# Kernel optimization log

Hardware: AMD Instinct MI355X
Metric: run time of the kernel (lower is better)

The kernel has to match this reference:

```python
import jax, jax.numpy as jnp
import numpy as np

C = 256
C8 = C // 8
B, H, W = 4, 64, 64


def setup_inputs() -> dict:
    key = jax.random.key(0)
    ks = jax.random.split(key, 8)
    s = 0.02
    return {
        "x": jax.random.normal(ks[0], (B, C, H, W), dtype=jnp.float32),
        "qw": jax.random.normal(ks[1], (C8, C), dtype=jnp.float32) * s,
        "qb": jax.random.normal(ks[2], (C8,), dtype=jnp.float32) * s,
        "kw": jax.random.normal(ks[3], (C8, C), dtype=jnp.float32) * s,
        "kb": jax.random.normal(ks[4], (C8,), dtype=jnp.float32) * s,
        "vw": jax.random.normal(ks[5], (C, C), dtype=jnp.float32) * s,
        "vb": jax.random.normal(ks[6], (C,), dtype=jnp.float32) * s,
        "gamma": jnp.full((1,), 0.1, dtype=jnp.float32),
    }


def reference(x, qw, qb, kw, kb, vw, vb, gamma):
    b, c, h, w = x.shape
    n = h * w
    xf = x.reshape(b, c, n)  # (B, C, N)
    # 1x1 convs == per-pixel linear projections
    q = jnp.einsum('dc,bcn->bnd', qw, xf) + qb  # (B, N, C/8)
    k = jnp.einsum('dc,bcn->bdn', kw, xf) + kb[None, :, None]  # (B, C/8, N)
    v = jnp.einsum('dc,bcn->bdn', vw, xf) + vb[None, :, None]  # (B, C, N)
    scores = jnp.einsum('bnd,bdm->bnm', q, k)  # (B, N, N), no scale (as in source)
    attn = jax.nn.softmax(scores, axis=-1)
    # out[b,c,i] = sum_j v[b,c,j] * attn[b,i,j]
    out = jnp.einsum('bcj,bij->bci', v, attn).reshape(b, c, h, w)
    return x + gamma.reshape(()) * out
```

## Files before the change

kernel.cpp:

```cpp
#include <hip/hip_runtime.h>
#include <hip/hip_bf16.h>
#include <math.h>

#define CC 256
#define NN 4096

typedef __bf16 bf16x8 __attribute__((ext_vector_type(8)));
typedef __bf16 bf16x4 __attribute__((ext_vector_type(4)));
typedef float  f32x4  __attribute__((ext_vector_type(4)));

#define MFMA16x16x32 __builtin_amdgcn_mfma_f32_16x16x32_bf16

__device__ inline float exp2_hw(float x) {
    float r;
    asm("v_exp_f32 %0, %1" : "=v"(r) : "v"(x));
    return r;
}

__device__ inline int kperm(int j) {
    return ((j & 12) << 1) | ((j & 16) >> 2) | (j & 3);
}

__global__ void wprep_kernel(
    const float* __restrict__ qw, const float* __restrict__ qb,
    const float* __restrict__ kw, const float* __restrict__ kb,
    const float* __restrict__ vw, const float* __restrict__ vb,
    __bf16* __restrict__ Wh, __bf16* __restrict__ Wl, float* __restrict__ biasF)
{
    const int r = blockIdx.x;
    const int c = threadIdx.x;
    const float L2E = 1.4426950408889634f;
    const float* wsrc; const float* bsrc; int r0; float scale;
    if (r < 32)       { wsrc = qw; bsrc = qb; r0 = r;      scale = L2E; }
    else if (r < 64)  { wsrc = kw; bsrc = kb; r0 = r - 32; scale = 1.f; }
    else              { wsrc = vw; bsrc = vb; r0 = r - 64; scale = 1.f; }
    float v = wsrc[(size_t)r0 * CC + c] * scale;
    __bf16 hi = (__bf16)v;
    Wh[(size_t)r * CC + c] = hi;
    Wl[(size_t)r * CC + c] = (__bf16)(v - (float)hi);
    if (c == 0) biasF[r] = bsrc[r0] * scale;
}

__global__ __launch_bounds__(512) void proj_kernel(
    const float* __restrict__ x,
    const __bf16* __restrict__ Wh, const __bf16* __restrict__ Wl,
    const float* __restrict__ biasF,
    __bf16* __restrict__ Qb, __bf16* __restrict__ Kb, __bf16* __restrict__ V2)
{
    const int t    = threadIdx.x;
    const int w    = t >> 6;
    const int lane = t & 63;
    const int lrow = lane & 15;
    const int lgrp = lane >> 4;
    const int n0   = blockIdx.x * 64;
    const int b    = blockIdx.y;
    const int nt   = w & 3;
    const int rp   = w >> 2;

    __shared__ float  xs[64][68];
    __shared__ __bf16 xbh[64][136];
    __shared__ __bf16 xbl[64][136];

    f32x4 acc[10];
    #pragma unroll
    for (int i = 0; i < 10; ++i) acc[i] = f32x4{0.f, 0.f, 0.f, 0.f};

    for (int ch = 0; ch < 2; ++ch) {
        for (int cc = 0; cc < 2; ++cc) {
            __syncthreads();
            {
                const float* xg = x + ((size_t)b * CC + ch * 128 + cc * 64) * NN + n0;
                const int row = t >> 3;
                const int col = (t & 7) * 8;
                float4 a0 = *(const float4*)&xg[(size_t)row * NN + col];
                float4 a1 = *(const float4*)&xg[(size_t)row * NN + col + 4];
                *(float4*)&xs[row][col]     = a0;
                *(float4*)&xs[row][col + 4] = a1;
            }
            __syncthreads();
            {
                const int cn = t & 63;
                const int cg = t >> 6;
                bf16x8 h, l;
                #pragma unroll
                for (int e = 0; e < 8; ++e) {
                    float v = xs[cg * 8 + e][cn];
                    __bf16 hi = (__bf16)v;
                    h[e] = hi; l[e] = (__bf16)(v - (float)hi);
                }
                *(bf16x8*)&xbh[cn][cc * 64 + cg * 8] = h;
                *(bf16x8*)&xbl[cn][cc * 64 + cg * 8] = l;
            }
        }
        __syncthreads();

        #pragma unroll
        for (int ks = 0; ks < 4; ++ks) {
            const bf16x8 bh = *(const bf16x8*)&xbh[nt * 16 + lrow][ks * 32 + lgrp * 8];
            const bf16x8 bl = *(const bf16x8*)&xbl[nt * 16 + lrow][ks * 32 + lgrp * 8];
            #pragma unroll
            for (int i = 0; i < 10; ++i) {
                const int rt = rp + 2 * i;
                const size_t ao = (size_t)(rt * 16 + lrow) * CC + ch * 128 + ks * 32 + lgrp * 8;
                const bf16x8 ah = *(const bf16x8*)&Wh[ao];
                const bf16x8 al = *(const bf16x8*)&Wl[ao];
                acc[i] = MFMA16x16x32(ah, bh, acc[i], 0, 0, 0);
                acc[i] = MFMA16x16x32(ah, bl, acc[i], 0, 0, 0);
                acc[i] = MFMA16x16x32(al, bh, acc[i], 0, 0, 0);
            }
        }
    }

    const int n = n0 + nt * 16 + lrow;
    #pragma unroll
    for (int i = 0; i < 10; ++i) {
        const int rt = rp + 2 * i;
        const int g0 = rt * 16 + lgrp * 4;
        const float4 b4 = *(const float4*)&biasF[g0];
        const float v0 = acc[i].x + b4.x, v1 = acc[i].y + b4.y;
        const float v2 = acc[i].z + b4.z, v3 = acc[i].w + b4.w;
        if (g0 < 32) {
            bf16x4 o = { (__bf16)v0, (__bf16)v1, (__bf16)v2, (__bf16)v3 };
            *(bf16x4*)&Qb[((size_t)b * NN + n) * 32 + g0] = o;
        } else if (g0 < 64) {
            bf16x4 o = { (__bf16)v0, (__bf16)v1, (__bf16)v2, (__bf16)v3 };
            *(bf16x4*)&Kb[((size_t)b * NN + n) * 32 + (g0 - 32)] = o;
        } else {
            const int c = g0 - 64;
            const size_t base = ((size_t)b * 128 + (n >> 5)) * (CC * 32) + kperm(n & 31);
            V2[base + (size_t)(c + 0) * 32] = (__bf16)v0;
            V2[base + (size_t)(c + 1) * 32] = (__bf16)v1;
            V2[base + (size_t)(c + 2) * 32] = (__bf16)v2;
            V2[base + (size_t)(c + 3) * 32] = (__bf16)v3;
        }
    }
}

__global__ __launch_bounds__(512, 2) void attn_kernel(
    const __bf16* __restrict__ Qb, const __bf16* __restrict__ Kb,
    const __bf16* __restrict__ V2,
    const float* __restrict__ x, const float* __restrict__ gamma,
    float* __restrict__ y)
{
    const int bid  = blockIdx.x;
    const int xcd  = bid & 7;
    const int b    = xcd >> 1;
    const int qt   = (xcd & 1) * 32 + (bid >> 3);
    const int w    = threadIdx.x >> 6;
    const int lane = threadIdx.x & 63;
    const int lrow = lane & 15;
    const int lgrp = lane >> 4;
    const int qg   = w >> 1;
    const int kh   = w & 1;
    const int c0w  = w * 32;

    __shared__ __align__(16) __bf16 P[2][64][64];
    __shared__ float lsumP[64][2];

    const __bf16* Qbb = Qb + (size_t)b * NN * 32;
    const __bf16* Kbb = Kb + (size_t)b * NN * 32;
    const __bf16* Vbb = V2 + (size_t)b * 128 * (CC * 32);

    const bf16x8 qf = *(const bf16x8*)&Qbb[(size_t)(qt * 64 + qg * 16 + lrow) * 32 + lgrp * 8];

    const size_t koff0 = (size_t)(kh * 32 + lrow) * 32 + lgrp * 8;
    const size_t koff1 = koff0 + 16 * 32;
    const size_t vbase = (size_t)(c0w + lrow) * 32 + lgrp * 8;

    f32x4 Oa[4], Ob[4];
    #pragma unroll
    for (int g2 = 0; g2 < 4; ++g2) { Oa[g2] = f32x4{0.f,0.f,0.f,0.f}; Ob[g2] = f32x4{0.f,0.f,0.f,0.f}; }
    float lsum_l = 0.f;
    const f32x4 zf = f32x4{0.f, 0.f, 0.f, 0.f};

    const int swz  = 16 * (lrow & 7);
    char* prow_w   = (char*)&P[0][qg * 16 + lrow][0];
    const int woff = (kh * 64 + 16 * lgrp) ^ swz;

    bf16x8 kf0 = *(const bf16x8*)&Kbb[koff0];
    bf16x8 kf1 = *(const bf16x8*)&Kbb[koff1];

    for (int jt = 0; jt < 64; ++jt) {
        const size_t vrow = ((size_t)(2 * jt)) * (CC * 32) + vbase;
        const bf16x8 vf00 = *(const bf16x8*)&Vbb[vrow];
        const bf16x8 vf01 = *(const bf16x8*)&Vbb[vrow + 16 * 32];
        const bf16x8 vf10 = *(const bf16x8*)&Vbb[vrow + (size_t)(CC * 32)];
        const bf16x8 vf11 = *(const bf16x8*)&Vbb[vrow + (size_t)(CC * 32) + 16 * 32];
        const size_t jn = (size_t)((jt + 1) & 63) * 64 * 32;
        const bf16x8 kn0 = *(const bf16x8*)&Kbb[jn + koff0];
        const bf16x8 kn1 = *(const bf16x8*)&Kbb[jn + koff1];

        const f32x4 s0 = MFMA16x16x32(kf0, qf, zf, 0, 0, 0);
        const f32x4 s1 = MFMA16x16x32(kf1, qf, zf, 0, 0, 0);

        float ps = 0.f;
        bf16x8 pk;
        #pragma unroll
        for (int r = 0; r < 4; ++r) { float e = exp2_hw(s0[r]); ps += e; pk[r]     = (__bf16)e; }
        #pragma unroll
        for (int r = 0; r < 4; ++r) { float e = exp2_hw(s1[r]); ps += e; pk[4 + r] = (__bf16)e; }
        lsum_l += ps;

        const int buf = jt & 1;
        *(bf16x8*)(prow_w + buf * 8192 + woff) = pk;

        asm volatile("s_waitcnt lgkmcnt(0)\n\ts_barrier" ::: "memory");

        #pragma unroll
        for (int g2 = 0; g2 < 4; ++g2) {
            const char* prow_r = (const char*)&P[buf][g2 * 16 + lrow][0];
            const bf16x8 pb0 = *(const bf16x8*)(prow_r + ((16 * lgrp) ^ swz));
            const bf16x8 pb1 = *(const bf16x8*)(prow_r + ((64 + 16 * lgrp) ^ swz));
            Oa[g2] = MFMA16x16x32(vf00, pb0, Oa[g2], 0, 0, 0);
            Oa[g2] = MFMA16x16x32(vf10, pb1, Oa[g2], 0, 0, 0);
            Ob[g2] = MFMA16x16x32(vf01, pb0, Ob[g2], 0, 0, 0);
            Ob[g2] = MFMA16x16x32(vf11, pb1, Ob[g2], 0, 0, 0);
        }
        kf0 = kn0; kf1 = kn1;
    }

    lsum_l += __shfl_xor(lsum_l, 16);
    lsum_l += __shfl_xor(lsum_l, 32);
    if (lgrp == 0) lsumP[qg * 16 + lrow][kh] = lsum_l;
    __syncthreads();

    const float gm = gamma[0];
    #pragma unroll
    for (int g2 = 0; g2 < 4; ++g2) {
        const int q = qt * 64 + g2 * 16 + lrow;
        const float rinv = 1.f / (lsumP[g2 * 16 + lrow][0] + lsumP[g2 * 16 + lrow][1]);
        #pragma unroll
        for (int r = 0; r < 4; ++r) {
            const int c0 = c0w + lgrp * 4 + r;
            const size_t i0 = ((size_t)b * CC + c0) * NN + q;
            y[i0] = x[i0] + gm * Oa[g2][r] * rinv;
            const size_t i1 = ((size_t)b * CC + c0 + 16) * NN + q;
            y[i1] = x[i1] + gm * Ob[g2][r] * rinv;
        }
    }
}

extern "C" void kernel_launch(void* const* d_in, const int* in_sizes, int n_in,
                              void* d_out, int out_size, void* d_ws, size_t ws_size,
                              hipStream_t stream)
{
    const float* x     = (const float*)d_in[0];
    const float* qw    = (const float*)d_in[1];
    const float* qb    = (const float*)d_in[2];
    const float* kw    = (const float*)d_in[3];
    const float* kb    = (const float*)d_in[4];
    const float* vw    = (const float*)d_in[5];
    const float* vb    = (const float*)d_in[6];
    const float* gamma = (const float*)d_in[7];
    float* y = (float*)d_out;

    char* ws = (char*)d_ws;
    __bf16* Wh    = (__bf16*)(ws);
    __bf16* Wl    = (__bf16*)(ws + 163840);
    float*  biasF = (float*) (ws + 327680);
    __bf16* Qb    = (__bf16*)(ws + 1048576);
    __bf16* Kb    = (__bf16*)(ws + 2097152);
    __bf16* V2    = (__bf16*)(ws + 3145728);

    hipLaunchKernelGGL(wprep_kernel, dim3(320), dim3(256), 0, stream,
                       qw, qb, kw, kb, vw, vb, Wh, Wl, biasF);
    hipLaunchKernelGGL(proj_kernel, dim3(64, 4), dim3(512), 0, stream,
                       x, Wh, Wl, biasF, Qb, Kb, V2);
    hipLaunchKernelGGL(attn_kernel, dim3(256), dim3(512), 0, stream,
                       Qb, Kb, V2, x, gamma, y);
}
```

Measured before the change: 178.2 us.

## Split projection rows and attention channels across twice as many blocks

The projection kernel now splits its 320 output rows into two halves over a new grid dimension, halving each block's accumulators. The attention kernel splits the 256 value channels into two halves per query tile, doubling the grid to 512 blocks and raising the occupancy hint to 4 blocks per CU. Each attention block now redoes the QK^T scores and exponentials for its half of the channels. The aim is more parallelism and occupancy on the GPU's CUs, at the cost of computing the softmax twice.

Result: slower. 187.7 us (+5.3%).

```diff
diff --git a/kernel.cpp b/kernel.cpp
--- a/kernel.cpp
+++ b/kernel.cpp
@@ -53,7 +53,8 @@
     const int lrow = lane & 15;
     const int lgrp = lane >> 4;
     const int n0   = blockIdx.x * 64;
-    const int b    = blockIdx.y;
+    const int rh   = blockIdx.y;
+    const int b    = blockIdx.z;
     const int nt   = w & 3;
     const int rp   = w >> 2;
 
@@ -61,9 +62,9 @@
     __shared__ __bf16 xbh[64][136];
     __shared__ __bf16 xbl[64][136];
 
-    f32x4 acc[10];
-    #pragma unroll
-    for (int i = 0; i < 10; ++i) acc[i] = f32x4{0.f, 0.f, 0.f, 0.f};
+    f32x4 acc[5];
+    #pragma unroll
+    for (int i = 0; i < 5; ++i) acc[i] = f32x4{0.f, 0.f, 0.f, 0.f};
 
     for (int ch = 0; ch < 2; ++ch) {
         for (int cc = 0; cc < 2; ++cc) {
@@ -99,9 +100,9 @@
             const bf16x8 bh = *(const bf16x8*)&xbh[nt * 16 + lrow][ks * 32 + lgrp * 8];
             const bf16x8 bl = *(const bf16x8*)&xbl[nt * 16 + lrow][ks * 32 + lgrp * 8];
             #pragma unroll
-            for (int i = 0; i < 10; ++i) {
+            for (int i = 0; i < 5; ++i) {
                 const int rt = rp + 2 * i;
-                const size_t ao = (size_t)(rt * 16 + lrow) * CC + ch * 128 + ks * 32 + lgrp * 8;
+                const size_t ao = (size_t)(rh * 160 + rt * 16 + lrow) * CC + ch * 128 + ks * 32 + lgrp * 8;
                 const bf16x8 ah = *(const bf16x8*)&Wh[ao];
                 const bf16x8 al = *(const bf16x8*)&Wl[ao];
                 acc[i] = MFMA16x16x32(ah, bh, acc[i], 0, 0, 0);
@@ -113,9 +114,9 @@
 
     const int n = n0 + nt * 16 + lrow;
     #pragma unroll
-    for (int i = 0; i < 10; ++i) {
+    for (int i = 0; i < 5; ++i) {
         const int rt = rp + 2 * i;
-        const int g0 = rt * 16 + lgrp * 4;
+        const int g0 = rh * 160 + rt * 16 + lgrp * 4;
         const float4 b4 = *(const float4*)&biasF[g0];
         const float v0 = acc[i].x + b4.x, v1 = acc[i].y + b4.y;
         const float v2 = acc[i].z + b4.z, v3 = acc[i].w + b4.w;
@@ -136,7 +137,7 @@
     }
 }
 
-__global__ __launch_bounds__(512, 2) void attn_kernel(
+__global__ __launch_bounds__(512, 4) void attn_kernel(
     const __bf16* __restrict__ Qb, const __bf16* __restrict__ Kb,
     const __bf16* __restrict__ V2,
     const float* __restrict__ x, const float* __restrict__ gamma,
@@ -145,48 +146,48 @@
     const int bid  = blockIdx.x;
     const int xcd  = bid & 7;
     const int b    = xcd >> 1;
-    const int qt   = (xcd & 1) * 32 + (bid >> 3);
+    const int hh   = xcd & 1;
+    const int qt   = bid >> 3;
     const int w    = threadIdx.x >> 6;
     const int lane = threadIdx.x & 63;
     const int lrow = lane & 15;
     const int lgrp = lane >> 4;
     const int qg   = w >> 1;
     const int kh   = w & 1;
-    const int c0w  = w * 32;
+    const int c0w  = hh * 128 + w * 16;
 
     __shared__ __align__(16) __bf16 P[2][64][64];
     __shared__ float lsumP[64][2];
 
     const __bf16* Qbb = Qb + (size_t)b * NN * 32;
     const __bf16* Kbb = Kb + (size_t)b * NN * 32;
-    const __bf16* Vbb = V2 + (size_t)b * 128 * (CC * 32);
+    const __bf16* Vbb = V2 + (size_t)b * 128 * 8192;
 
     const bf16x8 qf = *(const bf16x8*)&Qbb[(size_t)(qt * 64 + qg * 16 + lrow) * 32 + lgrp * 8];
 
     const size_t koff0 = (size_t)(kh * 32 + lrow) * 32 + lgrp * 8;
-    const size_t koff1 = koff0 + 16 * 32;
-    const size_t vbase = (size_t)(c0w + lrow) * 32 + lgrp * 8;
-
-    f32x4 Oa[4], Ob[4];
-    #pragma unroll
-    for (int g2 = 0; g2 < 4; ++g2) { Oa[g2] = f32x4{0.f,0.f,0.f,0.f}; Ob[g2] = f32x4{0.f,0.f,0.f,0.f}; }
+    const size_t koff1 = koff0 + 512;
+    const size_t voff0 = (size_t)(c0w + lrow) * 32 + lgrp * 8;
+    const size_t voff1 = voff0 + 8192;
+
+    f32x4 O[4];
+    #pragma unroll
+    for (int g2 = 0; g2 < 4; ++g2) O[g2] = f32x4{0.f, 0.f, 0.f, 0.f};
     float lsum_l = 0.f;
     const f32x4 zf = f32x4{0.f, 0.f, 0.f, 0.f};
 
     const int swz  = 16 * (lrow & 7);
-    char* prow_w   = (char*)&P[0][qg * 16 + lrow][0];
+    char* prowW    = (char*)&P[0][qg * 16 + lrow][0];
     const int woff = (kh * 64 + 16 * lgrp) ^ swz;
 
     bf16x8 kf0 = *(const bf16x8*)&Kbb[koff0];
     bf16x8 kf1 = *(const bf16x8*)&Kbb[koff1];
 
     for (int jt = 0; jt < 64; ++jt) {
-        const size_t vrow = ((size_t)(2 * jt)) * (CC * 32) + vbase;
-        const bf16x8 vf00 = *(const bf16x8*)&Vbb[vrow];
-        const bf16x8 vf01 = *(const bf16x8*)&Vbb[vrow + 16 * 32];
-        const bf16x8 vf10 = *(const bf16x8*)&Vbb[vrow + (size_t)(CC * 32)];
-        const bf16x8 vf11 = *(const bf16x8*)&Vbb[vrow + (size_t)(CC * 32) + 16 * 32];
-        const size_t jn = (size_t)((jt + 1) & 63) * 64 * 32;
+        const size_t vrow = (size_t)(2 * jt) * 8192;
+        const bf16x8 vf0 = *(const bf16x8*)&Vbb[vrow + voff0];
+        const bf16x8 vf1 = *(const bf16x8*)&Vbb[vrow + voff1];
+        const size_t jn = (size_t)((jt + 1) & 63) * 2048;
         const bf16x8 kn0 = *(const bf16x8*)&Kbb[jn + koff0];
         const bf16x8 kn1 = *(const bf16x8*)&Kbb[jn + koff1];
 
@@ -202,19 +203,17 @@
         lsum_l += ps;
 
         const int buf = jt & 1;
-        *(bf16x8*)(prow_w + buf * 8192 + woff) = pk;
+        *(bf16x8*)(prowW + buf * 8192 + woff) = pk;
 
         asm volatile("s_waitcnt lgkmcnt(0)\n\ts_barrier" ::: "memory");
 
         #pragma unroll
         for (int g2 = 0; g2 < 4; ++g2) {
-            const char* prow_r = (const char*)&P[buf][g2 * 16 + lrow][0];
-            const bf16x8 pb0 = *(const bf16x8*)(prow_r + ((16 * lgrp) ^ swz));
-            const bf16x8 pb1 = *(const bf16x8*)(prow_r + ((64 + 16 * lgrp) ^ swz));
-            Oa[g2] = MFMA16x16x32(vf00, pb0, Oa[g2], 0, 0, 0);
-            Oa[g2] = MFMA16x16x32(vf10, pb1, Oa[g2], 0, 0, 0);
-            Ob[g2] = MFMA16x16x32(vf01, pb0, Ob[g2], 0, 0, 0);
-            Ob[g2] = MFMA16x16x32(vf11, pb1, Ob[g2], 0, 0, 0);
+            const char* pr = (const char*)&P[buf][g2 * 16 + lrow][0];
+            const bf16x8 pb0 = *(const bf16x8*)(pr + ((16 * lgrp) ^ swz));
+            const bf16x8 pb1 = *(const bf16x8*)(pr + ((64 + 16 * lgrp) ^ swz));
+            O[g2] = MFMA16x16x32(vf0, pb0, O[g2], 0, 0, 0);
+            O[g2] = MFMA16x16x32(vf1, pb1, O[g2], 0, 0, 0);
         }
         kf0 = kn0; kf1 = kn1;
     }
@@ -231,11 +230,9 @@
         const float rinv = 1.f / (lsumP[g2 * 16 + lrow][0] + lsumP[g2 * 16 + lrow][1]);
         #pragma unroll
         for (int r = 0; r < 4; ++r) {
-            const int c0 = c0w + lgrp * 4 + r;
-            const size_t i0 = ((size_t)b * CC + c0) * NN + q;
-            y[i0] = x[i0] + gm * Oa[g2][r] * rinv;
-            const size_t i1 = ((size_t)b * CC + c0 + 16) * NN + q;
-            y[i1] = x[i1] + gm * Ob[g2][r] * rinv;
+            const int c = c0w + lgrp * 4 + r;
+            const size_t idx = ((size_t)b * CC + c) * NN + q;
+            y[idx] = x[idx] + gm * O[g2][r] * rinv;
         }
     }
 }
@@ -264,8 +261,8 @@
 
     hipLaunchKernelGGL(wprep_kernel, dim3(320), dim3(256), 0, stream,
                        qw, qb, kw, kb, vw, vb, Wh, Wl, biasF);
-    hipLaunchKernelGGL(proj_kernel, dim3(64, 4), dim3(512), 0, stream,
+    hipLaunchKernelGGL(proj_kernel, dim3(64, 2, 4), dim3(512), 0, stream,
                        x, Wh, Wl, biasF, Qb, Kb, V2);
-    hipLaunchKernelGGL(attn_kernel, dim3(256), dim3(512), 0, stream,
+    hipLaunchKernelGGL(attn_kernel, dim3(512), dim3(512), 0, stream,
                        Qb, Kb, V2, x, gamma, y);
 }
```
